# Kernel tuning notes

Hardware: AMD Instinct MI355X
Metric: run time of the kernel (lower is better)

Reference implementation:

```python
import jax, jax.numpy as jnp
import numpy as np

NEG_BIG = -2.0**32 + 1.0

def setup_inputs() -> dict:
    key = jax.random.key(0)
    ks = jax.random.split(key, 8)
    B, T, D = 4096, 200, 32
    H1, H2 = 80, 40
    s = lambda n: 1.0 / np.sqrt(n)
    return {
        "q": jax.random.normal(ks[0], (B, D), jnp.float32),
        "k": jax.random.normal(ks[1], (B, T, D), jnp.float32),
        "v": jax.random.normal(ks[2], (B, T, D), jnp.float32),
        "mask": jax.random.randint(ks[3], (B, T), 0, 2, jnp.int32),
        "Wq": jax.random.normal(ks[4], (D, D), jnp.float32) * s(D),
        "bq": jnp.zeros((D,), jnp.float32),
        "alpha": jnp.zeros((D,), jnp.float32),  # Keras PReLU default alpha=0
        "W1": jax.random.normal(ks[5], (4 * D, H1), jnp.float32) * s(4 * D),
        "b1": jnp.zeros((H1,), jnp.float32),
        "W2": jax.random.normal(ks[6], (H1, H2), jnp.float32) * s(H1),
        "b2": jnp.zeros((H2,), jnp.float32),
        "Wf": jax.random.normal(ks[7], (H2, 1), jnp.float32) * s(H2),
        "bf": jnp.zeros((1,), jnp.float32),
    }

def prelu(x, a):
    return jnp.where(x >= 0, x, a * x)

def reference(q, k, v, mask, Wq, bq, alpha, W1, b1, W2, b2, Wf, bf):
    # dense_q with PReLU activation: [B, D] -> [B, 32]
    qp = prelu(q @ Wq + bq, alpha)
    # tile query across history steps: [B, T, 32]
    qt = jnp.broadcast_to(qp[:, None, :], k.shape)
    # DIN attention features: [B, T, 4*32]
    info = jnp.concatenate([qt, k, qt - k, qt * k], axis=-1)
    info = jax.nn.sigmoid(info @ W1 + b1)
    info = jax.nn.sigmoid(info @ W2 + b2)
    logits = (info @ Wf + bf).squeeze(-1)  # [B, T]
    logits = jnp.where(mask == 0, jnp.full_like(logits, NEG_BIG), logits)
    att = jax.nn.softmax(logits, axis=-1)
    return att[:, None, :]  # [B, 1, T]
```

## Files before the change

kernel.cpp:

```cpp
#include <hip/hip_runtime.h>
#include <math.h>

typedef float f32x4 __attribute__((ext_vector_type(4)));
typedef _Float16 f16;
typedef f16 f16x8 __attribute__((ext_vector_type(8)));
typedef unsigned int u32;
typedef u32 u32x2 __attribute__((ext_vector_type(2)));

#define BB 4096
#define TT 200
#define DD 32
#define H1 80
#define H2 40
#define SLAB_W 104

__device__ __align__(16) float g_BCj[DD * H1];
__device__ __align__(16) float g_Dj [DD * H1];
__device__ __align__(16) float g_ACj[DD * H1];
__device__ __align__(16) f16 g_w2h[9 * 64 * 8];

__device__ __forceinline__ float fast_sigmoid(float x) {
    return __builtin_amdgcn_rcpf(1.f + __expf(-x));
}

__global__ void pack_kernel(const float* __restrict__ W1, const float* __restrict__ W2) {
    int idx = blockIdx.x * 256 + threadIdx.x;
    if (idx < DD * H1) {
        int kk = idx / H1, j = idx % H1;
        g_BCj[idx] = W1[(32 + kk) * H1 + j] - W1[(64 + kk) * H1 + j];
        g_Dj [idx] = W1[(96 + kk) * H1 + j];
        g_ACj[idx] = W1[kk * H1 + j] + W1[(64 + kk) * H1 + j];
        return;
    }
    idx -= DD * H1;
    if (idx < 9 * 64 * 8) {
        int e = idx & 7, l = (idx >> 3) & 63, g = idx >> 9;
        int kt = g / 3, n = g % 3;
        int j   = kt * 32 + (l >> 4) * 8 + e;
        int col = n * 16 + (l & 15);
        float v = (j < H1 && col < H2) ? W2[j * H2 + col] : 0.f;
        g_w2h[idx] = (f16)v;
    }
}

__global__ __launch_bounds__(256) void din_mfma(
    const float* __restrict__ q, const float* __restrict__ k, const int* __restrict__ mask,
    const float* __restrict__ Wq, const float* __restrict__ bq, const float* __restrict__ alpha,
    const float* __restrict__ b1, const float* __restrict__ b2, const float* __restrict__ Wf,
    float* __restrict__ out)
{
    const int tid = threadIdx.x;
    const int wid = tid >> 6, l = tid & 63;
    const int l15 = l & 15, lg4 = l >> 4;
    const int b   = (blockIdx.x << 2) | wid;

    __shared__ __align__(16) f16   slab[4][16][SLAB_W];
    __shared__ __align__(16) float qp_s[4][DD];
    __shared__ __align__(16) float u_s[4][H1];
    __shared__ __align__(16) float lgt[4][208];

    const int* mrow = mask + (size_t)b * TT;
    int mk0 = mrow[l];
    int mk1 = mrow[64 + l];
    int mk2 = mrow[128 + l];
    int mk3 = (l < 8) ? mrow[192 + l] : 1;

    if (l < DD) {
        const float* qr = q + (size_t)b * DD;
        float acc = bq[l];
        #pragma unroll
        for (int e = 0; e < DD; ++e) acc += qr[e] * Wq[e * DD + l];
        float a = alpha[l];
        qp_s[wid][l] = acc >= 0.f ? acc : a * acc;
    }
    {
        u32* wsz = (u32*)slab[wid];
        #pragma unroll
        for (int i = 0; i < 2; ++i) {
            int idx = i * 64 + l;
            wsz[(idx >> 3) * 52 + 40 + (idx & 7)] = 0u;
        }
    }

    #pragma unroll
    for (int i = 0; i < 2; ++i) {
        int c = i * 64 + l;
        if (c < H1) {
            float acc = b1[c];
            #pragma unroll
            for (int d = 0; d < DD; ++d) acc += qp_s[wid][d] * g_ACj[d * H1 + c];
            u_s[wid][c] = acc;
        }
    }
    f16x8 Bh[5], Bl[5];
    #pragma unroll
    for (int n = 0; n < 5; ++n) {
        #pragma unroll
        for (int e = 0; e < 8; ++e) {
            int kidx = lg4 * 8 + e;
            int j = n * 16 + l15;
            float v = g_BCj[kidx * H1 + j] + qp_s[wid][kidx] * g_Dj[kidx * H1 + j];
            f16 hi = (f16)v;
            Bh[n][e] = hi;
            Bl[n][e] = (f16)(v - (float)hi);
        }
    }
    f16x8 W2h[9];
    #pragma unroll
    for (int g = 0; g < 9; ++g) W2h[g] = *(const f16x8*)(g_w2h + (g * 64 + l) * 8);
    float blr[3], wlr[3];
    #pragma unroll
    for (int n = 0; n < 3; ++n) {
        int col = n * 16 + l15;
        blr[n] = col < H2 ? b2[col] : 0.f;
        wlr[n] = col < H2 ? Wf[col] : 0.f;
    }

    const float* kb = k + (size_t)b * (TT * DD);
    f16 (*ws)[SLAB_W] = slab[wid];
    float* lg = lgt[wid];

    f32x4 x0, x1;
    {
        const f32x4* kr = (const f32x4*)(kb + l15 * DD + lg4 * 8);
        x0 = kr[0]; x1 = kr[1];
    }

    for (int m = 0; m < 13; ++m) {
        f16x8 Ah;
        #pragma unroll
        for (int e = 0; e < 4; ++e) {
            Ah[e]     = (f16)x0[e];
            Ah[e + 4] = (f16)x1[e];
        }
        if (m < 12) {
            int tn = (m + 1) * 16 + l15; if (tn > TT - 1) tn = TT - 1;
            const f32x4* kr = (const f32x4*)(kb + tn * DD + lg4 * 8);
            x0 = kr[0]; x1 = kr[1];
        }

        #pragma unroll
        for (int n = 0; n < 5; ++n) {
            int j0 = n * 16 + lg4 * 4;
            f32x4 acc = *(const f32x4*)(&u_s[wid][j0]);
            acc = __builtin_amdgcn_mfma_f32_16x16x32_f16(Bh[n], Ah, acc, 0, 0, 0);
            acc = __builtin_amdgcn_mfma_f32_16x16x32_f16(Bl[n], Ah, acc, 0, 0, 0);
            auto p01 = __builtin_amdgcn_cvt_pkrtz(fast_sigmoid(acc[0]), fast_sigmoid(acc[1]));
            auto p23 = __builtin_amdgcn_cvt_pkrtz(fast_sigmoid(acc[2]), fast_sigmoid(acc[3]));
            u32x2 w;
            w[0] = __builtin_bit_cast(u32, p01);
            w[1] = __builtin_bit_cast(u32, p23);
            *(u32x2*)(&ws[l15][j0]) = w;
        }

        f32x4 a0 = {0.f,0.f,0.f,0.f}, a1 = {0.f,0.f,0.f,0.f}, a2 = {0.f,0.f,0.f,0.f};
        #pragma unroll
        for (int kt = 0; kt < 3; ++kt) {
            f16x8 sh = *(const f16x8*)(&ws[l15][kt * 32 + lg4 * 8]);
            a0 = __builtin_amdgcn_mfma_f32_16x16x32_f16(sh, W2h[kt * 3 + 0], a0, 0, 0, 0);
            a1 = __builtin_amdgcn_mfma_f32_16x16x32_f16(sh, W2h[kt * 3 + 1], a1, 0, 0, 0);
            a2 = __builtin_amdgcn_mfma_f32_16x16x32_f16(sh, W2h[kt * 3 + 2], a2, 0, 0, 0);
        }
        float p0 = 0.f, p1 = 0.f, p2 = 0.f, p3 = 0.f;
        #pragma unroll
        for (int n = 0; n < 3; ++n) {
            f32x4 av = (n == 0) ? a0 : (n == 1) ? a1 : a2;
            p0 += wlr[n] * fast_sigmoid(av[0] + blr[n]);
            p1 += wlr[n] * fast_sigmoid(av[1] + blr[n]);
            p2 += wlr[n] * fast_sigmoid(av[2] + blr[n]);
            p3 += wlr[n] * fast_sigmoid(av[3] + blr[n]);
        }
        #pragma unroll
        for (int off = 1; off < 16; off <<= 1) {
            p0 += __shfl_xor(p0, off);
            p1 += __shfl_xor(p1, off);
            p2 += __shfl_xor(p2, off);
            p3 += __shfl_xor(p3, off);
        }
        if (l15 == 0) {
            int tb = m * 16 + lg4 * 4;
            lg[tb + 0] = p0; lg[tb + 1] = p1; lg[tb + 2] = p2; lg[tb + 3] = p3;
        }
    }

    const float NEG = -4294967295.0f;
    float v0 = lg[l];        if (mk0 == 0) v0 = NEG;
    float v1 = lg[64 + l];   if (mk1 == 0) v1 = NEG;
    float v2 = lg[128 + l];  if (mk2 == 0) v2 = NEG;
    float v3 = -8589934590.0f;
    if (l < 8) { v3 = lg[192 + l]; if (mk3 == 0) v3 = NEG; }

    float mx = fmaxf(fmaxf(v0, v1), fmaxf(v2, v3));
    #pragma unroll
    for (int off = 32; off; off >>= 1) mx = fmaxf(mx, __shfl_xor(mx, off));

    float e0 = __expf(v0 - mx), e1 = __expf(v1 - mx);
    float e2 = __expf(v2 - mx), e3 = __expf(v3 - mx);
    float s = (e0 + e1) + (e2 + e3);
    #pragma unroll
    for (int off = 32; off; off >>= 1) s += __shfl_xor(s, off);

    float* orow = out + (size_t)b * TT;
    orow[l]       = e0 / s;
    orow[64 + l]  = e1 / s;
    orow[128 + l] = e2 / s;
    if (l < 8) orow[192 + l] = e3 / s;
}

extern "C" void kernel_launch(void* const* d_in, const int* in_sizes, int n_in,
                              void* d_out, int out_size, void* d_ws, size_t ws_size,
                              hipStream_t stream) {
    const float* q     = (const float*)d_in[0];
    const float* k     = (const float*)d_in[1];
    const int*   mask  = (const int*)d_in[3];
    const float* Wq    = (const float*)d_in[4];
    const float* bq    = (const float*)d_in[5];
    const float* alpha = (const float*)d_in[6];
    const float* W1    = (const float*)d_in[7];
    const float* b1    = (const float*)d_in[8];
    const float* W2    = (const float*)d_in[9];
    const float* b2    = (const float*)d_in[10];
    const float* Wf    = (const float*)d_in[11];
    float* out = (float*)d_out;

    hipLaunchKernelGGL(pack_kernel, dim3((DD * H1 + 9 * 64 * 8 + 255) / 256), dim3(256),
                       0, stream, W1, W2);
    hipLaunchKernelGGL(din_mfma, dim3(BB / 4), dim3(256), 0, stream,
                       q, k, mask, Wq, bq, alpha, b1, b2, Wf, out);
}
```

Baseline: 53.67 us.

## Software-pipeline layer-1 and layer-2 MFMAs with double-buffered LDS slab

Double-buffers the per-wave hidden-activation slab so layer 1 for tile m+1 is computed while layer 2 consumes tile m, letting the two MFMA chains and the sigmoid work interleave. The k prefetch moves two tiles ahead. It also adds a minimum of 4 blocks per CU to launch_bounds to constrain register use. The cost is doubled slab LDS and more live registers, which may cause spills under the tighter launch bound.

Result: slower. 79.74 us (+48.6%).

```diff
diff --git a/kernel.cpp b/kernel.cpp
--- a/kernel.cpp
+++ b/kernel.cpp
@@ -43,7 +43,7 @@
     }
 }
 
-__global__ __launch_bounds__(256) void din_mfma(
+__global__ __launch_bounds__(256, 4) void din_mfma(
     const float* __restrict__ q, const float* __restrict__ k, const int* __restrict__ mask,
     const float* __restrict__ Wq, const float* __restrict__ bq, const float* __restrict__ alpha,
     const float* __restrict__ b1, const float* __restrict__ b2, const float* __restrict__ Wf,
@@ -54,7 +54,7 @@
     const int l15 = l & 15, lg4 = l >> 4;
     const int b   = (blockIdx.x << 2) | wid;
 
-    __shared__ __align__(16) f16   slab[4][16][SLAB_W];
+    __shared__ __align__(16) f16   slab[4][2][16][SLAB_W];
     __shared__ __align__(16) float qp_s[4][DD];
     __shared__ __align__(16) float u_s[4][H1];
     __shared__ __align__(16) float lgt[4][208];
@@ -74,11 +74,14 @@
         qp_s[wid][l] = acc >= 0.f ? acc : a * acc;
     }
     {
-        u32* wsz = (u32*)slab[wid];
+        u32* z0 = (u32*)slab[wid][0];
+        u32* z1 = (u32*)slab[wid][1];
         #pragma unroll
         for (int i = 0; i < 2; ++i) {
             int idx = i * 64 + l;
-            wsz[(idx >> 3) * 52 + 40 + (idx & 7)] = 0u;
+            int off = (idx >> 3) * 52 + 40 + (idx & 7);
+            z0[off] = 0u;
+            z1[off] = 0u;
         }
     }
 
@@ -117,28 +120,25 @@
     }
 
     const float* kb = k + (size_t)b * (TT * DD);
-    f16 (*ws)[SLAB_W] = slab[wid];
+    f16 (*ws0)[SLAB_W] = slab[wid][0];
+    f16 (*ws1)[SLAB_W] = slab[wid][1];
     float* lg = lgt[wid];
 
     f32x4 x0, x1;
-    {
-        const f32x4* kr = (const f32x4*)(kb + l15 * DD + lg4 * 8);
+    auto loadk = [&](int m) {
+        int t = m * 16 + l15; if (t > TT - 1) t = TT - 1;
+        const f32x4* kr = (const f32x4*)(kb + t * DD + lg4 * 8);
         x0 = kr[0]; x1 = kr[1];
-    }
-
-    for (int m = 0; m < 13; ++m) {
+    };
+
+    auto l1_full = [&](f16 (*wbuf)[SLAB_W], int nload) {
         f16x8 Ah;
         #pragma unroll
         for (int e = 0; e < 4; ++e) {
             Ah[e]     = (f16)x0[e];
             Ah[e + 4] = (f16)x1[e];
         }
-        if (m < 12) {
-            int tn = (m + 1) * 16 + l15; if (tn > TT - 1) tn = TT - 1;
-            const f32x4* kr = (const f32x4*)(kb + tn * DD + lg4 * 8);
-            x0 = kr[0]; x1 = kr[1];
-        }
-
+        if (nload >= 0) loadk(nload);
         #pragma unroll
         for (int n = 0; n < 5; ++n) {
             int j0 = n * 16 + lg4 * 4;
@@ -150,17 +150,28 @@
             u32x2 w;
             w[0] = __builtin_bit_cast(u32, p01);
             w[1] = __builtin_bit_cast(u32, p23);
-            *(u32x2*)(&ws[l15][j0]) = w;
-        }
+            *(u32x2*)(&wbuf[l15][j0]) = w;
+        }
+    };
+
+    auto body = [&](int m, f16 (*rbuf)[SLAB_W], f16 (*wbuf)[SLAB_W]) {
+        f16x8 sh0 = *(const f16x8*)(&rbuf[l15][0 * 32 + lg4 * 8]);
+        f16x8 sh1 = *(const f16x8*)(&rbuf[l15][1 * 32 + lg4 * 8]);
+        f16x8 sh2 = *(const f16x8*)(&rbuf[l15][2 * 32 + lg4 * 8]);
+
+        if (m < 12) l1_full(wbuf, m < 11 ? m + 2 : -1);
 
         f32x4 a0 = {0.f,0.f,0.f,0.f}, a1 = {0.f,0.f,0.f,0.f}, a2 = {0.f,0.f,0.f,0.f};
-        #pragma unroll
-        for (int kt = 0; kt < 3; ++kt) {
-            f16x8 sh = *(const f16x8*)(&ws[l15][kt * 32 + lg4 * 8]);
-            a0 = __builtin_amdgcn_mfma_f32_16x16x32_f16(sh, W2h[kt * 3 + 0], a0, 0, 0, 0);
-            a1 = __builtin_amdgcn_mfma_f32_16x16x32_f16(sh, W2h[kt * 3 + 1], a1, 0, 0, 0);
-            a2 = __builtin_amdgcn_mfma_f32_16x16x32_f16(sh, W2h[kt * 3 + 2], a2, 0, 0, 0);
-        }
+        a0 = __builtin_amdgcn_mfma_f32_16x16x32_f16(sh0, W2h[0], a0, 0, 0, 0);
+        a1 = __builtin_amdgcn_mfma_f32_16x16x32_f16(sh0, W2h[1], a1, 0, 0, 0);
+        a2 = __builtin_amdgcn_mfma_f32_16x16x32_f16(sh0, W2h[2], a2, 0, 0, 0);
+        a0 = __builtin_amdgcn_mfma_f32_16x16x32_f16(sh1, W2h[3], a0, 0, 0, 0);
+        a1 = __builtin_amdgcn_mfma_f32_16x16x32_f16(sh1, W2h[4], a1, 0, 0, 0);
+        a2 = __builtin_amdgcn_mfma_f32_16x16x32_f16(sh1, W2h[5], a2, 0, 0, 0);
+        a0 = __builtin_amdgcn_mfma_f32_16x16x32_f16(sh2, W2h[6], a0, 0, 0, 0);
+        a1 = __builtin_amdgcn_mfma_f32_16x16x32_f16(sh2, W2h[7], a1, 0, 0, 0);
+        a2 = __builtin_amdgcn_mfma_f32_16x16x32_f16(sh2, W2h[8], a2, 0, 0, 0);
+
         float p0 = 0.f, p1 = 0.f, p2 = 0.f, p3 = 0.f;
         #pragma unroll
         for (int n = 0; n < 3; ++n) {
@@ -181,6 +192,14 @@
             int tb = m * 16 + lg4 * 4;
             lg[tb + 0] = p0; lg[tb + 1] = p1; lg[tb + 2] = p2; lg[tb + 3] = p3;
         }
+    };
+
+    loadk(0);
+    l1_full(ws0, 1);
+
+    for (int m = 0; m < 13; m += 2) {
+        body(m, ws0, ws1);
+        if (m + 1 < 13) body(m + 1, ws1, ws0);
     }
 
     const float NEG = -4294967295.0f;
```
